# Optimization experiments

Measured on AMD Instinct MI355X. Metric: run time of the kernel, lower is better.

## Reference

```python
import jax, jax.numpy as jnp
import numpy as np

N = 100000
E = 1600000
IN_DIM = 128
HID = 64
HEADS = 4
OUT = HID // HEADS  # 16
LAYERS = 3
NEG_SLOPE = 0.2
LN_EPS = 1e-5


def setup_inputs() -> dict:
    key = jax.random.key(0)
    ks = jax.random.split(key, 12)
    x = jax.random.normal(ks[0], (N, IN_DIM), dtype=jnp.float32)
    edge_index = jax.random.randint(ks[1], (2, E), 0, N, dtype=jnp.int32)
    s = 0.05
    Win = jax.random.normal(ks[2], (IN_DIM, HID), dtype=jnp.float32) * s
    bin_ = jnp.zeros((HID,), dtype=jnp.float32)
    Wg = jax.random.normal(ks[3], (LAYERS, HID, HEADS * OUT), dtype=jnp.float32) * s
    att_src = jax.random.normal(ks[4], (LAYERS, HEADS, OUT), dtype=jnp.float32) * s
    att_dst = jax.random.normal(ks[5], (LAYERS, HEADS, OUT), dtype=jnp.float32) * s
    bg = jnp.zeros((LAYERS, HID), dtype=jnp.float32)
    ln_g = jnp.ones((LAYERS, HID), dtype=jnp.float32)
    ln_b = jnp.zeros((LAYERS, HID), dtype=jnp.float32)
    Wout = jax.random.normal(ks[6], (HID, 1), dtype=jnp.float32) * s
    bout = jnp.zeros((1,), dtype=jnp.float32)
    return {"x": x, "edge_index": edge_index, "Win": Win, "bin_": bin_,
            "Wg": Wg, "att_src": att_src, "att_dst": att_dst, "bg": bg,
            "ln_g": ln_g, "ln_b": ln_b, "Wout": Wout, "bout": bout}


def _gat_layer(x, src, dst, W, a_s, a_d, b):
    # x: [N, HID]; linear transform then split heads
    h = (x @ W).reshape(N, HEADS, OUT)                       # [N,H,C]
    alpha_s = jnp.einsum('nhc,hc->nh', h, a_s)               # [N,H]
    alpha_d = jnp.einsum('nhc,hc->nh', h, a_d)               # [N,H]
    e = alpha_s[src] + alpha_d[dst]                          # [E',H]
    e = jnp.where(e > 0, e, NEG_SLOPE * e)                   # LeakyReLU(0.2)
    # segment softmax over destination node
    m = jax.ops.segment_max(e, dst, num_segments=N)          # [N,H]
    ee = jnp.exp(e - m[dst])
    z = jax.ops.segment_sum(ee, dst, num_segments=N)         # [N,H]
    alpha = ee / (z[dst] + 1e-16)                            # [E',H]
    msg = alpha[:, :, None] * h[src]                         # [E',H,C]
    out = jax.ops.segment_sum(msg, dst, num_segments=N)      # [N,H,C]
    return out.reshape(N, HID) + b


def _layer_norm(x, g, b):
    mu = jnp.mean(x, axis=-1, keepdims=True)
    var = jnp.mean(jnp.square(x - mu), axis=-1, keepdims=True)
    return (x - mu) * jax.lax.rsqrt(var + LN_EPS) * g + b


def reference(x, edge_index, Win, bin_, Wg, att_src, att_dst, bg, ln_g, ln_b, Wout, bout):
    # add self loops (PyG GATConv default)
    loops = jnp.arange(N, dtype=edge_index.dtype)
    src = jnp.concatenate([edge_index[0], loops])
    dst = jnp.concatenate([edge_index[1], loops])
    h = jax.nn.relu(x @ Win + bin_)                          # input_proj + ReLU
    for i in range(LAYERS):
        res = h
        h = _gat_layer(h, src, dst, Wg[i], att_src[i], att_dst[i], bg[i])
        h = _layer_norm(h, ln_g[i], ln_b[i])
        h = jax.nn.relu(h)
        h = h + res                                          # dropout is identity in eval
    out = h @ Wout + bout                                    # [N,1]
    return out.reshape(-1)
```

## Files before the change

kernel.cpp:

```cpp
#include <hip/hip_runtime.h>
#include <hip/hip_bf16.h>

#define N_NODES 100000
#define E_EDGES 1600000
#define IN_DIM  128
#define HID     64
#define HEADS   4
#define NEG_SLOPE 0.2f
#define LN_EPS  1e-5f
#define LOG2E   1.4426950408889634f

#define BUCK_SHIFT 7
#define NODES_PER_BUCK 128
#define NBUCK ((N_NODES + NODES_PER_BUCK - 1) / NODES_PER_BUCK)
#define NBUCK_PAD 1024
#define PART_CHUNK 4096

__device__ __forceinline__ float bflo(unsigned u) { return __uint_as_float(u << 16); }
__device__ __forceinline__ float bfhi(unsigned u) { return __uint_as_float(u & 0xffff0000u); }
__device__ __forceinline__ unsigned packbf2(float a, float b) {
    unsigned ua = __float_as_uint(a), ub = __float_as_uint(b);
    ua += 0x7fffu + ((ua >> 16) & 1u);
    ub += 0x7fffu + ((ub >> 16) & 1u);
    return (ua >> 16) | (ub & 0xffff0000u);
}
__device__ __forceinline__ float lrexp2(float e) {
    return __builtin_amdgcn_exp2f(fmaxf(e, NEG_SLOPE * e));
}

__global__ __launch_bounds__(256) void k_in_proj(
        const float* __restrict__ x, const float* __restrict__ W,
        const float* __restrict__ bias, float* __restrict__ h) {
    __shared__ float Xs[32][132];
    __shared__ float Ws[128][64];
    int t = threadIdx.x;
    const float4* W4 = (const float4*)W;
    float4* Ws4 = (float4*)&Ws[0][0];
    #pragma unroll
    for (int i = 0; i < 8; ++i) Ws4[t + 256 * i] = W4[t + 256 * i];
    int base = blockIdx.x * 32;
    const float4* X4 = (const float4*)(x + (size_t)base * IN_DIM);
    #pragma unroll
    for (int i = 0; i < 4; ++i) {
        int f = t + 256 * i;
        int row = f >> 5, col4 = f & 31;
        ((float4*)&Xs[row][0])[col4] = X4[f];
    }
    __syncthreads();
    int r = t >> 4;
    int c = (t & 15) * 4;
    float4 bb = *(const float4*)(bias + c);
    float4 acc0 = bb, acc1 = bb;
    #pragma unroll 8
    for (int k = 0; k < 128; ++k) {
        float a0 = Xs[r][k];
        float a1 = Xs[r + 16][k];
        float4 b = *(const float4*)&Ws[k][c];
        acc0.x += a0 * b.x; acc0.y += a0 * b.y; acc0.z += a0 * b.z; acc0.w += a0 * b.w;
        acc1.x += a1 * b.x; acc1.y += a1 * b.y; acc1.z += a1 * b.z; acc1.w += a1 * b.w;
    }
    acc0.x = fmaxf(acc0.x, 0.f); acc0.y = fmaxf(acc0.y, 0.f);
    acc0.z = fmaxf(acc0.z, 0.f); acc0.w = fmaxf(acc0.w, 0.f);
    acc1.x = fmaxf(acc1.x, 0.f); acc1.y = fmaxf(acc1.y, 0.f);
    acc1.z = fmaxf(acc1.z, 0.f); acc1.w = fmaxf(acc1.w, 0.f);
    *(float4*)(h + (size_t)(base + r) * HID + c) = acc0;
    *(float4*)(h + (size_t)(base + r + 16) * HID + c) = acc1;
}

__global__ __launch_bounds__(256) void k_gat_lin(
        const float* __restrict__ h, const float* __restrict__ W,
        const float* __restrict__ as_w, const float* __restrict__ ad_w,
        unsigned* __restrict__ hlb, float* __restrict__ as_o, float* __restrict__ ad_o) {
    __shared__ float Xs[32][68];
    __shared__ float Ws[64][64];
    int t = threadIdx.x;
    const float4* W4 = (const float4*)W;
    float4* Ws4 = (float4*)&Ws[0][0];
    #pragma unroll
    for (int i = 0; i < 4; ++i) Ws4[t + 256 * i] = W4[t + 256 * i];
    int base = blockIdx.x * 32;
    const float4* X4 = (const float4*)(h + (size_t)base * HID);
    #pragma unroll
    for (int i = 0; i < 2; ++i) {
        int f = t + 256 * i;
        int row = f >> 4, col4 = f & 15;
        ((float4*)&Xs[row][0])[col4] = X4[f];
    }
    __syncthreads();
    int r = t >> 4;
    int c = (t & 15) * 4;
    float4 acc0 = {0.f, 0.f, 0.f, 0.f}, acc1 = {0.f, 0.f, 0.f, 0.f};
    #pragma unroll 8
    for (int k = 0; k < 64; ++k) {
        float a0 = Xs[r][k];
        float a1 = Xs[r + 16][k];
        float4 b = *(const float4*)&Ws[k][c];
        acc0.x += a0 * b.x; acc0.y += a0 * b.y; acc0.z += a0 * b.z; acc0.w += a0 * b.w;
        acc1.x += a1 * b.x; acc1.y += a1 * b.y; acc1.z += a1 * b.z; acc1.w += a1 * b.w;
    }
    uint2 p0, p1;
    p0.x = packbf2(acc0.x, acc0.y); p0.y = packbf2(acc0.z, acc0.w);
    p1.x = packbf2(acc1.x, acc1.y); p1.y = packbf2(acc1.z, acc1.w);
    ((uint2*)hlb)[(size_t)(base + r) * 16 + (c >> 2)] = p0;
    ((uint2*)hlb)[(size_t)(base + r + 16) * 16 + (c >> 2)] = p1;
    float4 A = *(const float4*)(as_w + c);
    float4 D = *(const float4*)(ad_w + c);
    A.x *= LOG2E; A.y *= LOG2E; A.z *= LOG2E; A.w *= LOG2E;
    D.x *= LOG2E; D.y *= LOG2E; D.z *= LOG2E; D.w *= LOG2E;
    float s0 = acc0.x * A.x + acc0.y * A.y + acc0.z * A.z + acc0.w * A.w;
    float d0 = acc0.x * D.x + acc0.y * D.y + acc0.z * D.z + acc0.w * D.w;
    float s1 = acc1.x * A.x + acc1.y * A.y + acc1.z * A.z + acc1.w * A.w;
    float d1 = acc1.x * D.x + acc1.y * D.y + acc1.z * D.z + acc1.w * D.w;
    #pragma unroll
    for (int off = 1; off < 4; off <<= 1) {
        s0 += __shfl_xor(s0, off); d0 += __shfl_xor(d0, off);
        s1 += __shfl_xor(s1, off); d1 += __shfl_xor(d1, off);
    }
    if ((t & 3) == 0) {
        int head = (t & 15) >> 2;
        as_o[(size_t)(base + r) * HEADS + head] = s0;
        ad_o[(size_t)(base + r) * HEADS + head] = d0;
        as_o[(size_t)(base + r + 16) * HEADS + head] = s1;
        ad_o[(size_t)(base + r + 16) * HEADS + head] = d1;
    }
}

__global__ __launch_bounds__(256) void k_bhist(const int* __restrict__ dstp,
                                               int* __restrict__ bcnt) {
    __shared__ int c[NBUCK_PAD];
    int t = threadIdx.x;
    for (int i = t; i < NBUCK_PAD; i += 256) c[i] = 0;
    __syncthreads();
    for (int i = blockIdx.x * 256 + t; i < E_EDGES; i += gridDim.x * 256)
        atomicAdd(&c[dstp[i] >> BUCK_SHIFT], 1);
    __syncthreads();
    for (int i = t; i < NBUCK_PAD; i += 256) {
        int v = c[i];
        if (v) atomicAdd(bcnt + i, v);
    }
}

__global__ __launch_bounds__(1024) void k_bscan(const int* __restrict__ bcnt,
                                                int* __restrict__ bbase,
                                                int* __restrict__ bcur) {
    __shared__ int s[NBUCK_PAD];
    int tid = threadIdx.x;
    int v = bcnt[tid];
    s[tid] = v;
    __syncthreads();
    for (int off = 1; off < NBUCK_PAD; off <<= 1) {
        int t = (tid >= off) ? s[tid - off] : 0;
        __syncthreads();
        s[tid] += t;
        __syncthreads();
    }
    int excl = s[tid] - v;
    bbase[tid] = excl;
    bcur[tid] = excl;
    if (tid == NBUCK_PAD - 1) bbase[NBUCK_PAD] = s[tid];
}

__global__ __launch_bounds__(256) void k_part(const int* __restrict__ srcp,
                                              const int* __restrict__ dstp,
                                              int* __restrict__ bcur,
                                              int2* __restrict__ ebuf) {
    __shared__ int cnt[NBUCK_PAD];
    __shared__ int gbase[NBUCK_PAD];
    int t = threadIdx.x;
    for (int i = t; i < NBUCK_PAD; i += 256) cnt[i] = 0;
    int e0 = blockIdx.x * PART_CHUNK;
    int e1 = min(e0 + PART_CHUNK, E_EDGES);
    __syncthreads();
    for (int i = e0 + t; i < e1; i += 256)
        atomicAdd(&cnt[dstp[i] >> BUCK_SHIFT], 1);
    __syncthreads();
    for (int b = t; b < NBUCK_PAD; b += 256) {
        int c = cnt[b];
        gbase[b] = c ? atomicAdd(bcur + b, c) : 0;
        cnt[b] = 0;
    }
    __syncthreads();
    for (int i = e0 + t; i < e1; i += 256) {
        int d = dstp[i];
        int b = d >> BUCK_SHIFT;
        int pos = gbase[b] + atomicAdd(&cnt[b], 1);
        ebuf[pos] = make_int2(srcp[i], d);
    }
}

__global__ __launch_bounds__(256) void k_fin(const int* __restrict__ bbase,
                                             const int2* __restrict__ ebuf,
                                             int* __restrict__ row,
                                             int* __restrict__ ssrc) {
    __shared__ int cnt[NODES_PER_BUCK];
    __shared__ int sc[NODES_PER_BUCK];
    __shared__ int rbase[NODES_PER_BUCK];
    int t = threadIdx.x;
    int b = blockIdx.x;
    int start = bbase[b], end = bbase[b + 1];
    int nb0 = b << BUCK_SHIFT;
    if (t < NODES_PER_BUCK) cnt[t] = 0;
    __syncthreads();
    for (int i = start + t; i < end; i += 256)
        atomicAdd(&cnt[ebuf[i].y - nb0], 1);
    __syncthreads();
    if (t < NODES_PER_BUCK) sc[t] = cnt[t];
    __syncthreads();
    for (int off = 1; off < NODES_PER_BUCK; off <<= 1) {
        int v = (t < NODES_PER_BUCK && t >= off) ? sc[t - off] : 0;
        __syncthreads();
        if (t < NODES_PER_BUCK) sc[t] += v;
        __syncthreads();
    }
    if (t < NODES_PER_BUCK) {
        int rb = start + sc[t] - cnt[t];
        rbase[t] = rb;
        int n = nb0 + t;
        if (n < N_NODES) row[n] = rb;
        cnt[t] = 0;
    }
    if (b == NBUCK - 1 && t == 0) row[N_NODES] = E_EDGES;
    __syncthreads();
    for (int i = start + t; i < end; i += 256) {
        int2 p = ebuf[i];
        int l = p.y - nb0;
        int slot = rbase[l] + atomicAdd(&cnt[l], 1);
        ssrc[slot] = p.x;
    }
}

__global__ __launch_bounds__(256) void k_gat_agg(
        const int* __restrict__ row, const int* __restrict__ ssrc,
        const float* __restrict__ as_, const float* __restrict__ ad_,
        const unsigned* __restrict__ hlb, const float* __restrict__ hres,
        const float* __restrict__ bg, const float* __restrict__ g,
        const float* __restrict__ b, float* __restrict__ hout,
        const float* __restrict__ Wout, const float* __restrict__ bout,
        float* __restrict__ out, int last) {
    int gid = blockIdx.x * blockDim.x + threadIdx.x;
    int n = gid >> 6;
    if (n >= N_NODES) return;
    int lane = threadIdx.x & 63;
    int grp = lane >> 4;
    int q   = lane & 15;
    int head = q >> 2;
    const uint2* hlb2 = (const uint2*)hlb;
    float adh = ad_[n * 4 + head];
    float acc0 = 0.f, acc1 = 0.f, acc2 = 0.f, acc3 = 0.f, z = 0.f;
    if (grp == 0) {
        float w = lrexp2(as_[n * 4 + head] + adh);
        uint2 u = hlb2[(size_t)n * 16 + q];
        acc0 = w * bflo(u.x); acc1 = w * bfhi(u.x);
        acc2 = w * bflo(u.y); acc3 = w * bfhi(u.y);
        z = w;
    }
    int j = row[n] + grp;
    int jend = row[n + 1];
    for (; j + 4 < jend; j += 8) {
        int s0 = ssrc[j], s1 = ssrc[j + 4];
        float wa = lrexp2(as_[s0 * 4 + head] + adh);
        float wb = lrexp2(as_[s1 * 4 + head] + adh);
        uint2 ua = hlb2[(size_t)s0 * 16 + q];
        uint2 ub = hlb2[(size_t)s1 * 16 + q];
        acc0 += wa * bflo(ua.x) + wb * bflo(ub.x);
        acc1 += wa * bfhi(ua.x) + wb * bfhi(ub.x);
        acc2 += wa * bflo(ua.y) + wb * bflo(ub.y);
        acc3 += wa * bfhi(ua.y) + wb * bfhi(ub.y);
        z += wa + wb;
    }
    if (j < jend) {
        int s0 = ssrc[j];
        float wa = lrexp2(as_[s0 * 4 + head] + adh);
        uint2 ua = hlb2[(size_t)s0 * 16 + q];
        acc0 += wa * bflo(ua.x);
        acc1 += wa * bfhi(ua.x);
        acc2 += wa * bflo(ua.y);
        acc3 += wa * bfhi(ua.y);
        z += wa;
    }
    acc0 += __shfl_xor(acc0, 16); acc0 += __shfl_xor(acc0, 32);
    acc1 += __shfl_xor(acc1, 16); acc1 += __shfl_xor(acc1, 32);
    acc2 += __shfl_xor(acc2, 16); acc2 += __shfl_xor(acc2, 32);
    acc3 += __shfl_xor(acc3, 16); acc3 += __shfl_xor(acc3, 32);
    z    += __shfl_xor(z, 16);    z    += __shfl_xor(z, 32);
    float rz = 1.f / (z + 1e-16f);
    float4 bgv = ((const float4*)bg)[q];
    float v0 = acc0 * rz + bgv.x;
    float v1 = acc1 * rz + bgv.y;
    float v2 = acc2 * rz + bgv.z;
    float v3 = acc3 * rz + bgv.w;
    float ssum = v0 + v1 + v2 + v3;
    #pragma unroll
    for (int off = 1; off < 16; off <<= 1) ssum += __shfl_xor(ssum, off);
    float mu = ssum * (1.f / 64.f);
    float d0 = v0 - mu, d1 = v1 - mu, d2 = v2 - mu, d3 = v3 - mu;
    float vs = d0 * d0 + d1 * d1 + d2 * d2 + d3 * d3;
    #pragma unroll
    for (int off = 1; off < 16; off <<= 1) vs += __shfl_xor(vs, off);
    float rstd = rsqrtf(vs * (1.f / 64.f) + LN_EPS);
    float4 gv = ((const float4*)g)[q];
    float4 bv = ((const float4*)b)[q];
    float4 hr = ((const float4*)hres)[(size_t)n * 16 + q];
    float y0 = fmaxf(d0 * rstd * gv.x + bv.x, 0.f) + hr.x;
    float y1 = fmaxf(d1 * rstd * gv.y + bv.y, 0.f) + hr.y;
    float y2 = fmaxf(d2 * rstd * gv.z + bv.z, 0.f) + hr.z;
    float y3 = fmaxf(d3 * rstd * gv.w + bv.w, 0.f) + hr.w;
    if (!last) {
        if (grp == 0) {
            float4 o; o.x = y0; o.y = y1; o.z = y2; o.w = y3;
            ((float4*)hout)[(size_t)n * 16 + q] = o;
        }
    } else {
        float4 wv = ((const float4*)Wout)[q];
        float pp = y0 * wv.x + y1 * wv.y + y2 * wv.z + y3 * wv.w;
        #pragma unroll
        for (int off = 1; off < 16; off <<= 1) pp += __shfl_xor(pp, off);
        if (lane == 0) out[n] = pp + bout[0];
    }
}

extern "C" void kernel_launch(void* const* d_in, const int* in_sizes, int n_in,
                              void* d_out, int out_size, void* d_ws, size_t ws_size,
                              hipStream_t stream) {
    const float* x     = (const float*)d_in[0];
    const int*   ei    = (const int*)  d_in[1];
    const float* Win   = (const float*)d_in[2];
    const float* bin_  = (const float*)d_in[3];
    const float* Wg    = (const float*)d_in[4];
    const float* att_s = (const float*)d_in[5];
    const float* att_d = (const float*)d_in[6];
    const float* bg    = (const float*)d_in[7];
    const float* lng   = (const float*)d_in[8];
    const float* lnb   = (const float*)d_in[9];
    const float* Wout  = (const float*)d_in[10];
    const float* bout  = (const float*)d_in[11];
    float* out = (float*)d_out;

    float* hA   = (float*)d_ws;
    float* hC   = hA + (size_t)N_NODES * 64;
    unsigned* hlb = (unsigned*)(hC + (size_t)N_NODES * 64);
    float* as_  = (float*)(hlb + (size_t)N_NODES * 32);
    float* ad_  = as_ + (size_t)N_NODES * 4;
    int* row    = (int*)(ad_ + (size_t)N_NODES * 4);
    int* bcnt   = row + (N_NODES + 1);
    int* bbase  = bcnt + NBUCK_PAD;
    int* bcur   = bbase + (NBUCK_PAD + 1);
    int* ssrc   = bcur + NBUCK_PAD;
    int2* ebuf  = (int2*)(ssrc + E_EDGES);

    const int* srcp = ei;
    const int* dstp = ei + E_EDGES;

    hipMemsetAsync(bcnt, 0, NBUCK_PAD * sizeof(int), stream);
    k_bhist<<<256, 256, 0, stream>>>(dstp, bcnt);
    k_bscan<<<1, NBUCK_PAD, 0, stream>>>(bcnt, bbase, bcur);
    k_part<<<(E_EDGES + PART_CHUNK - 1) / PART_CHUNK, 256, 0, stream>>>(srcp, dstp, bcur, ebuf);
    k_fin<<<NBUCK, 256, 0, stream>>>(bbase, ebuf, row, ssrc);

    k_in_proj<<<N_NODES / 32, 256, 0, stream>>>(x, Win, bin_, hA);

    const int aggBlocks = (N_NODES * 64 + 255) / 256;
    for (int L = 0; L < 3; ++L) {
        k_gat_lin<<<N_NODES / 32, 256, 0, stream>>>(hA, Wg + L * 64 * 64,
                                            att_s + L * 64, att_d + L * 64,
                                            hlb, as_, ad_);
        k_gat_agg<<<aggBlocks, 256, 0, stream>>>(row, ssrc, as_, ad_, hlb, hA,
                                                 bg + L * 64, lng + L * 64, lnb + L * 64,
                                                 hC, Wout, bout, out, (L == 2) ? 1 : 0);
        float* t = hA; hA = hC; hC = t;
    }
}
```

Before: 352.8 us.

## Fuse input projection with first GAT linear, pack edge buffer, use 32-bit gather offsets

The input projection kernel now also does the layer-0 GAT linear transform, writing the bf16 features and the attention logits directly, so one kernel launch and one re-read of h are removed. The partition buffer packs the source index and the local destination into a single 32-bit word instead of an int2, halving its traffic. The partition chunk size doubles, and the aggregation kernel computes gather addresses with 32-bit byte offsets. The fused kernel uses more shared memory, which may lower occupancy, and the packing assumes node ids fit in 17 bits.

Measured after the change: 354.9 us. Within noise of the previous version (+0.6%).

```diff
diff --git a/kernel.cpp b/kernel.cpp
--- a/kernel.cpp
+++ b/kernel.cpp
@@ -14,7 +14,7 @@
 #define NODES_PER_BUCK 128
 #define NBUCK ((N_NODES + NODES_PER_BUCK - 1) / NODES_PER_BUCK)
 #define NBUCK_PAD 1024
-#define PART_CHUNK 4096
+#define PART_CHUNK 8192
 
 __device__ __forceinline__ float bflo(unsigned u) { return __uint_as_float(u << 16); }
 __device__ __forceinline__ float bfhi(unsigned u) { return __uint_as_float(u & 0xffff0000u); }
@@ -28,16 +28,25 @@
     return __builtin_amdgcn_exp2f(fmaxf(e, NEG_SLOPE * e));
 }
 
-__global__ __launch_bounds__(256) void k_in_proj(
+__global__ __launch_bounds__(256) void k_in_proj_fused(
         const float* __restrict__ x, const float* __restrict__ W,
-        const float* __restrict__ bias, float* __restrict__ h) {
+        const float* __restrict__ bias,
+        const float* __restrict__ W2g, const float* __restrict__ as_w,
+        const float* __restrict__ ad_w,
+        float* __restrict__ h, unsigned* __restrict__ hlb,
+        float* __restrict__ as_o, float* __restrict__ ad_o) {
     __shared__ float Xs[32][132];
     __shared__ float Ws[128][64];
+    __shared__ float W2[64][64];
     int t = threadIdx.x;
     const float4* W4 = (const float4*)W;
     float4* Ws4 = (float4*)&Ws[0][0];
     #pragma unroll
     for (int i = 0; i < 8; ++i) Ws4[t + 256 * i] = W4[t + 256 * i];
+    const float4* W24 = (const float4*)W2g;
+    float4* W2s4 = (float4*)&W2[0][0];
+    #pragma unroll
+    for (int i = 0; i < 4; ++i) W2s4[t + 256 * i] = W24[t + 256 * i];
     int base = blockIdx.x * 32;
     const float4* X4 = (const float4*)(x + (size_t)base * IN_DIM);
     #pragma unroll
@@ -65,6 +74,45 @@
     acc1.z = fmaxf(acc1.z, 0.f); acc1.w = fmaxf(acc1.w, 0.f);
     *(float4*)(h + (size_t)(base + r) * HID + c) = acc0;
     *(float4*)(h + (size_t)(base + r + 16) * HID + c) = acc1;
+    __syncthreads();
+    float (*H2)[68] = (float(*)[68])Xs;
+    *(float4*)&H2[r][c] = acc0;
+    *(float4*)&H2[r + 16][c] = acc1;
+    __syncthreads();
+    float4 s0v = {0.f,0.f,0.f,0.f}, s1v = {0.f,0.f,0.f,0.f};
+    #pragma unroll 8
+    for (int k = 0; k < 64; ++k) {
+        float a0 = H2[r][k];
+        float a1 = H2[r + 16][k];
+        float4 b = *(const float4*)&W2[k][c];
+        s0v.x += a0 * b.x; s0v.y += a0 * b.y; s0v.z += a0 * b.z; s0v.w += a0 * b.w;
+        s1v.x += a1 * b.x; s1v.y += a1 * b.y; s1v.z += a1 * b.z; s1v.w += a1 * b.w;
+    }
+    uint2 p0, p1;
+    p0.x = packbf2(s0v.x, s0v.y); p0.y = packbf2(s0v.z, s0v.w);
+    p1.x = packbf2(s1v.x, s1v.y); p1.y = packbf2(s1v.z, s1v.w);
+    ((uint2*)hlb)[(size_t)(base + r) * 16 + (c >> 2)] = p0;
+    ((uint2*)hlb)[(size_t)(base + r + 16) * 16 + (c >> 2)] = p1;
+    float4 A = *(const float4*)(as_w + c);
+    float4 D = *(const float4*)(ad_w + c);
+    A.x *= LOG2E; A.y *= LOG2E; A.z *= LOG2E; A.w *= LOG2E;
+    D.x *= LOG2E; D.y *= LOG2E; D.z *= LOG2E; D.w *= LOG2E;
+    float s0 = s0v.x * A.x + s0v.y * A.y + s0v.z * A.z + s0v.w * A.w;
+    float d0 = s0v.x * D.x + s0v.y * D.y + s0v.z * D.z + s0v.w * D.w;
+    float s1 = s1v.x * A.x + s1v.y * A.y + s1v.z * A.z + s1v.w * A.w;
+    float d1 = s1v.x * D.x + s1v.y * D.y + s1v.z * D.z + s1v.w * D.w;
+    #pragma unroll
+    for (int off = 1; off < 4; off <<= 1) {
+        s0 += __shfl_xor(s0, off); d0 += __shfl_xor(d0, off);
+        s1 += __shfl_xor(s1, off); d1 += __shfl_xor(d1, off);
+    }
+    if ((t & 3) == 0) {
+        int head = (t & 15) >> 2;
+        as_o[(size_t)(base + r) * HEADS + head] = s0;
+        ad_o[(size_t)(base + r) * HEADS + head] = d0;
+        as_o[(size_t)(base + r + 16) * HEADS + head] = s1;
+        ad_o[(size_t)(base + r + 16) * HEADS + head] = d1;
+    }
 }
 
 __global__ __launch_bounds__(256) void k_gat_lin(
@@ -163,7 +211,7 @@
 __global__ __launch_bounds__(256) void k_part(const int* __restrict__ srcp,
                                               const int* __restrict__ dstp,
                                               int* __restrict__ bcur,
-                                              int2* __restrict__ ebuf) {
+                                              unsigned* __restrict__ ebuf) {
     __shared__ int cnt[NBUCK_PAD];
     __shared__ int gbase[NBUCK_PAD];
     int t = threadIdx.x;
@@ -184,12 +232,12 @@
         int d = dstp[i];
         int b = d >> BUCK_SHIFT;
         int pos = gbase[b] + atomicAdd(&cnt[b], 1);
-        ebuf[pos] = make_int2(srcp[i], d);
+        ebuf[pos] = (unsigned)srcp[i] | ((unsigned)(d & 127) << 17);
     }
 }
 
 __global__ __launch_bounds__(256) void k_fin(const int* __restrict__ bbase,
-                                             const int2* __restrict__ ebuf,
+                                             const unsigned* __restrict__ ebuf,
                                              int* __restrict__ row,
                                              int* __restrict__ ssrc) {
     __shared__ int cnt[NODES_PER_BUCK];
@@ -202,7 +250,7 @@
     if (t < NODES_PER_BUCK) cnt[t] = 0;
     __syncthreads();
     for (int i = start + t; i < end; i += 256)
-        atomicAdd(&cnt[ebuf[i].y - nb0], 1);
+        atomicAdd(&cnt[ebuf[i] >> 17], 1);
     __syncthreads();
     if (t < NODES_PER_BUCK) sc[t] = cnt[t];
     __syncthreads();
@@ -222,10 +270,10 @@
     if (b == NBUCK - 1 && t == 0) row[N_NODES] = E_EDGES;
     __syncthreads();
     for (int i = start + t; i < end; i += 256) {
-        int2 p = ebuf[i];
-        int l = p.y - nb0;
+        unsigned p = ebuf[i];
+        int l = (int)(p >> 17);
         int slot = rbase[l] + atomicAdd(&cnt[l], 1);
-        ssrc[slot] = p.x;
+        ssrc[slot] = (int)(p & 0x1FFFFu);
     }
 }
 
@@ -244,12 +292,15 @@
     int grp = lane >> 4;
     int q   = lane & 15;
     int head = q >> 2;
-    const uint2* hlb2 = (const uint2*)hlb;
+    const char* hlbc = (const char*)hlb;
+    const char* asc  = (const char*)as_;
+    unsigned qb = (unsigned)q * 8u;
+    unsigned hb = (unsigned)head * 4u;
     float adh = ad_[n * 4 + head];
     float acc0 = 0.f, acc1 = 0.f, acc2 = 0.f, acc3 = 0.f, z = 0.f;
     if (grp == 0) {
-        float w = lrexp2(as_[n * 4 + head] + adh);
-        uint2 u = hlb2[(size_t)n * 16 + q];
+        float w = lrexp2(*(const float*)(asc + ((unsigned)n * 16u + hb)) + adh);
+        uint2 u = *(const uint2*)(hlbc + ((unsigned)n * 128u + qb));
         acc0 = w * bflo(u.x); acc1 = w * bfhi(u.x);
         acc2 = w * bflo(u.y); acc3 = w * bfhi(u.y);
         z = w;
@@ -257,11 +308,11 @@
     int j = row[n] + grp;
     int jend = row[n + 1];
     for (; j + 4 < jend; j += 8) {
-        int s0 = ssrc[j], s1 = ssrc[j + 4];
-        float wa = lrexp2(as_[s0 * 4 + head] + adh);
-        float wb = lrexp2(as_[s1 * 4 + head] + adh);
-        uint2 ua = hlb2[(size_t)s0 * 16 + q];
-        uint2 ub = hlb2[(size_t)s1 * 16 + q];
+        unsigned s0 = (unsigned)ssrc[j], s1 = (unsigned)ssrc[j + 4];
+        float wa = lrexp2(*(const float*)(asc + (s0 * 16u + hb)) + adh);
+        float wb = lrexp2(*(const float*)(asc + (s1 * 16u + hb)) + adh);
+        uint2 ua = *(const uint2*)(hlbc + (s0 * 128u + qb));
+        uint2 ub = *(const uint2*)(hlbc + (s1 * 128u + qb));
         acc0 += wa * bflo(ua.x) + wb * bflo(ub.x);
         acc1 += wa * bfhi(ua.x) + wb * bfhi(ub.x);
         acc2 += wa * bflo(ua.y) + wb * bflo(ub.y);
@@ -269,9 +320,9 @@
         z += wa + wb;
     }
     if (j < jend) {
-        int s0 = ssrc[j];
-        float wa = lrexp2(as_[s0 * 4 + head] + adh);
-        uint2 ua = hlb2[(size_t)s0 * 16 + q];
+        unsigned s0 = (unsigned)ssrc[j];
+        float wa = lrexp2(*(const float*)(asc + (s0 * 16u + hb)) + adh);
+        uint2 ua = *(const uint2*)(hlbc + (s0 * 128u + qb));
         acc0 += wa * bflo(ua.x);
         acc1 += wa * bfhi(ua.x);
         acc2 += wa * bflo(ua.y);
@@ -346,7 +397,7 @@
     int* bbase  = bcnt + NBUCK_PAD;
     int* bcur   = bbase + (NBUCK_PAD + 1);
     int* ssrc   = bcur + NBUCK_PAD;
-    int2* ebuf  = (int2*)(ssrc + E_EDGES);
+    unsigned* ebuf = (unsigned*)(ssrc + E_EDGES);
 
     const int* srcp = ei;
     const int* dstp = ei + E_EDGES;
@@ -357,13 +408,16 @@
     k_part<<<(E_EDGES + PART_CHUNK - 1) / PART_CHUNK, 256, 0, stream>>>(srcp, dstp, bcur, ebuf);
     k_fin<<<NBUCK, 256, 0, stream>>>(bbase, ebuf, row, ssrc);
 
-    k_in_proj<<<N_NODES / 32, 256, 0, stream>>>(x, Win, bin_, hA);
+    k_in_proj_fused<<<N_NODES / 32, 256, 0, stream>>>(
+        x, Win, bin_, Wg, att_s, att_d, hA, hlb, as_, ad_);
 
     const int aggBlocks = (N_NODES * 64 + 255) / 256;
     for (int L = 0; L < 3; ++L) {
-        k_gat_lin<<<N_NODES / 32, 256, 0, stream>>>(hA, Wg + L * 64 * 64,
-                                            att_s + L * 64, att_d + L * 64,
-                                            hlb, as_, ad_);
+        if (L > 0) {
+            k_gat_lin<<<N_NODES / 32, 256, 0, stream>>>(hA, Wg + L * 64 * 64,
+                                                att_s + L * 64, att_d + L * 64,
+                                                hlb, as_, ad_);
+        }
         k_gat_agg<<<aggBlocks, 256, 0, stream>>>(row, ssrc, as_, ad_, hlb, hA,
                                                  bg + L * 64, lng + L * 64, lnb + L * 64,
                                                  hC, Wout, bout, out, (L == 2) ? 1 : 0);
```
